# Kernel tuning notes

Hardware: AMD Instinct MI355X
Metric: run time of the kernel (lower is better)

Reference implementation:

```python
import jax, jax.numpy as jnp
import numpy as np

B, H, V = 4096, 2048, 32000
IGNORE_INDEX = -100
BETA = 0.1


def setup_inputs() -> dict:
    key = jax.random.key(0)
    kx, kw, ky = jax.random.split(key, 3)
    x = jax.random.normal(kx, (B, H), dtype=jnp.float32)
    # nn.Linear weight: shape (V, H), uniform(-1/sqrt(H), 1/sqrt(H))
    bound = 1.0 / np.sqrt(H)
    W = jax.random.uniform(kw, (V, H), dtype=jnp.float32, minval=-bound, maxval=bound)
    y = jax.random.randint(ky, (B,), 0, V, dtype=jnp.int64)
    return {"x": x, "W": W, "y": y}


def reference(x, W, y):
    # Linear projection: (B,H) @ (H,V) -> (B,V)
    logits = jnp.einsum("bh,vh->bv", x, W)
    half = logits.shape[0] // 2

    # Cross entropy (mean reduction, ignore_index) on the chosen half.
    logp = jax.nn.log_softmax(logits[:half], axis=-1)  # (half, V)
    y_half = y[:half]
    valid = y_half != IGNORE_INDEX
    safe_y = jnp.where(valid, y_half, 0)
    nll = -jnp.take_along_axis(logp, safe_y[:, None], axis=-1)[:, 0]
    nll = jnp.where(valid, nll, 0.0)
    ce_loss = nll.sum() / jnp.maximum(valid.sum(), 1).astype(nll.dtype)

    # Mean log-prob over the vocab dim for every row (as in the reference).
    all_logprobs = jax.nn.log_softmax(logits, axis=-1).mean(axis=-1)  # (B,)
    chosen = all_logprobs[:half]
    rejected = all_logprobs[half:]

    # ORPO odds-ratio loss
    log_odds = (chosen - rejected) - (
        jnp.log1p(-jnp.exp(chosen)) - jnp.log1p(-jnp.exp(rejected))
    )
    or_losses = BETA * jax.nn.log_sigmoid(log_odds)
    return ce_loss - or_losses.mean()
```

## Files before the change

### kernel.cpp

```cpp
#include <hip/hip_runtime.h>
#include <stdint.h>

#define BDIM 4096
#define HDIM 2048
#define VDIM 32000
#define HALF (BDIM / 2)
#define IGNORE_INDEX (-100)

typedef int   v8i  __attribute__((ext_vector_type(8)));
typedef int   v4i  __attribute__((ext_vector_type(4)));
typedef float v16f __attribute__((ext_vector_type(16)));
typedef float f32x4 __attribute__((ext_vector_type(4)));
typedef __bf16 bf16x8 __attribute__((ext_vector_type(8)));

#define AS1 __attribute__((address_space(1)))
#define AS3 __attribute__((address_space(3)))

__device__ __forceinline__ unsigned short f2bf(float f) {
    union { float f; unsigned int u; } v; v.f = f;
    unsigned int u = v.u;
    unsigned int r = u + 0x7FFFu + ((u >> 16) & 1u);
    return (unsigned short)(r >> 16);
}

__global__ void cvt_fp8_kernel(const float* __restrict__ x,
                               const float* __restrict__ W,
                               uint8_t* __restrict__ xq,
                               uint8_t* __restrict__ wq,
                               int nx16, int ntot16) {
    int stride = gridDim.x * blockDim.x;
    for (int i = blockIdx.x * blockDim.x + threadIdx.x; i < ntot16; i += stride) {
        const float4* s; uint4* d; int j; float m;
        if (i < nx16) { s = (const float4*)x; d = (uint4*)xq; j = i; m = 1.0f; }
        else          { s = (const float4*)W; d = (uint4*)wq; j = i - nx16; m = 64.0f; }
        float4 f0 = s[4 * j + 0], f1 = s[4 * j + 1];
        float4 f2 = s[4 * j + 2], f3 = s[4 * j + 3];
        uint4 o; int w;
        w = __builtin_amdgcn_cvt_pk_fp8_f32(f0.x * m, f0.y * m, 0, false);
        w = __builtin_amdgcn_cvt_pk_fp8_f32(f0.z * m, f0.w * m, w, true);
        o.x = (unsigned)w;
        w = __builtin_amdgcn_cvt_pk_fp8_f32(f1.x * m, f1.y * m, 0, false);
        w = __builtin_amdgcn_cvt_pk_fp8_f32(f1.z * m, f1.w * m, w, true);
        o.y = (unsigned)w;
        w = __builtin_amdgcn_cvt_pk_fp8_f32(f2.x * m, f2.y * m, 0, false);
        w = __builtin_amdgcn_cvt_pk_fp8_f32(f2.z * m, f2.w * m, w, true);
        o.z = (unsigned)w;
        w = __builtin_amdgcn_cvt_pk_fp8_f32(f3.x * m, f3.y * m, 0, false);
        w = __builtin_amdgcn_cvt_pk_fp8_f32(f3.z * m, f3.w * m, w, true);
        o.w = (unsigned)w;
        d[j] = o;
    }
}

__global__ __launch_bounds__(256, 4)
void gemm_reduce_fp8(const uint8_t* __restrict__ A, const uint8_t* __restrict__ B,
                     const int* __restrict__ y,
                     float* __restrict__ sumexp, float* __restrict__ sumlog,
                     float* __restrict__ tlog) {
    __shared__ uint8_t sA[128 * 64];
    __shared__ uint8_t sB[128 * 64];

    const int tid = threadIdx.x;
    const int lane = tid & 63;
    const int wave = tid >> 6;
    const int wm = wave >> 1, wn = wave & 1;
    const int m0 = blockIdx.x * 128;
    const int v0 = blockIdx.y * 128;

    v16f acc[2][2];
#pragma unroll
    for (int i = 0; i < 2; i++)
#pragma unroll
        for (int j = 0; j < 2; j++)
#pragma unroll
            for (int r = 0; r < 16; r++) acc[i][j][r] = 0.f;

    const int srow = wave * 32 + (lane >> 2);
    const int sc   = ((lane & 3) - ((lane >> 3) & 3)) & 3;
    const uint8_t* gA0 = A + (size_t)(m0 + srow) * HDIM + sc * 16;
    const uint8_t* gB0 = B + (size_t)(v0 + srow) * HDIM + sc * 16;
    const uint8_t* gA1 = gA0 + (size_t)16 * HDIM;
    const uint8_t* gB1 = gB0 + (size_t)16 * HDIM;
    uint8_t* lA0 = &sA[(wave * 32) * 64];
    uint8_t* lA1 = lA0 + 16 * 64;
    uint8_t* lB0 = &sB[(wave * 32) * 64];
    uint8_t* lB1 = lB0 + 16 * 64;

    const int fr32 = lane & 31;
    const int h = lane >> 5;
    const int swr = (fr32 >> 1) & 3;
    const int pos0 = (2 * h + swr) & 3;
    const int pos1 = (2 * h + 1 + swr) & 3;
    const v4i* pA0 = (const v4i*)&sA[(wm * 64 + fr32) * 64];
    const v4i* pA1 = (const v4i*)&sA[(wm * 64 + 32 + fr32) * 64];
    const v4i* pB0 = (const v4i*)&sB[(wn * 64 + fr32) * 64];
    const v4i* pB1 = (const v4i*)&sB[(wn * 64 + 32 + fr32) * 64];

    for (int kt = 0; kt < HDIM; kt += 64) {
        __builtin_amdgcn_global_load_lds((const AS1 unsigned int*)(gA0 + kt),
                                         (AS3 unsigned int*)lA0, 16, 0, 0);
        __builtin_amdgcn_global_load_lds((const AS1 unsigned int*)(gA1 + kt),
                                         (AS3 unsigned int*)lA1, 16, 0, 0);
        __builtin_amdgcn_global_load_lds((const AS1 unsigned int*)(gB0 + kt),
                                         (AS3 unsigned int*)lB0, 16, 0, 0);
        __builtin_amdgcn_global_load_lds((const AS1 unsigned int*)(gB1 + kt),
                                         (AS3 unsigned int*)lB1, 16, 0, 0);
        __syncthreads();

        v4i a00 = pA0[pos0], a01 = pA0[pos1];
        v4i a10 = pA1[pos0], a11 = pA1[pos1];
        v4i b00 = pB0[pos0], b01 = pB0[pos1];
        v4i b10 = pB1[pos0], b11 = pB1[pos1];
        v8i af0 = {a00[0], a00[1], a00[2], a00[3], a01[0], a01[1], a01[2], a01[3]};
        v8i af1 = {a10[0], a10[1], a10[2], a10[3], a11[0], a11[1], a11[2], a11[3]};
        v8i bf0 = {b00[0], b00[1], b00[2], b00[3], b01[0], b01[1], b01[2], b01[3]};
        v8i bf1 = {b10[0], b10[1], b10[2], b10[3], b11[0], b11[1], b11[2], b11[3]};

        acc[0][0] = __builtin_amdgcn_mfma_scale_f32_32x32x64_f8f6f4(
            af0, bf0, acc[0][0], 0, 0, 0, 0x7F7F7F7F, 0, 0x7F7F7F7F);
        acc[0][1] = __builtin_amdgcn_mfma_scale_f32_32x32x64_f8f6f4(
            af0, bf1, acc[0][1], 0, 0, 0, 0x7F7F7F7F, 0, 0x7F7F7F7F);
        acc[1][0] = __builtin_amdgcn_mfma_scale_f32_32x32x64_f8f6f4(
            af1, bf0, acc[1][0], 0, 0, 0, 0x7F7F7F7F, 0, 0x7F7F7F7F);
        acc[1][1] = __builtin_amdgcn_mfma_scale_f32_32x32x64_f8f6f4(
            af1, bf1, acc[1][1], 0, 0, 0, 0x7F7F7F7F, 0, 0x7F7F7F7F);
        __syncthreads();
    }

    const float s64 = 0.015625f;
#pragma unroll
    for (int mi = 0; mi < 2; mi++) {
        const int baseRow = m0 + wm * 64 + mi * 32;
#pragma unroll
        for (int reg = 0; reg < 16; reg++) {
            float va = acc[mi][0][reg] * s64;
            float vb = acc[mi][1][reg] * s64;
            float e = __expf(va) + __expf(vb);
            float sm = va + vb;
#pragma unroll
            for (int off = 1; off < 32; off <<= 1) {
                e  += __shfl_xor(e, off);
                sm += __shfl_xor(sm, off);
            }
            int row = baseRow + (reg & 3) + 8 * (reg >> 2) + 4 * h;
            if (fr32 == 0) {
                atomicAdd(&sumexp[row], e);
                atomicAdd(&sumlog[row], sm);
            }
            int yv = y[row];
            int c0 = v0 + wn * 64 + fr32;
            if (c0 == yv) tlog[row] = va;
            if (c0 + 32 == yv) tlog[row] = vb;
        }
    }
}

__global__ __launch_bounds__(256, 4)
void gemm_reduce_f32(const float* __restrict__ A, const float* __restrict__ B,
                     const int* __restrict__ y,
                     float* __restrict__ sumexp, float* __restrict__ sumlog,
                     float* __restrict__ tlog) {
    __shared__ unsigned short sA[128 * 32];
    __shared__ unsigned short sB[128 * 32];

    const int tid  = threadIdx.x;
    const int lane = tid & 63;
    const int wave = tid >> 6;
    const int wm = wave >> 1, wn = wave & 1;
    const int m0 = blockIdx.x * 128;
    const int v0 = blockIdx.y * 128;
    const int fr = lane & 15;
    const int fq = lane >> 4;
    const int swz = (fr >> 1) & 3;

    f32x4 acc[4][4];
#pragma unroll
    for (int i = 0; i < 4; i++)
#pragma unroll
        for (int j = 0; j < 4; j++) acc[i][j] = (f32x4){0.f, 0.f, 0.f, 0.f};

    const int r8 = tid >> 3;
    const int kc = (tid & 7) * 4;
    for (int kt = 0; kt < HDIM; kt += 32) {
#pragma unroll
        for (int p = 0; p < 4; p++) {
            int row = p * 32 + r8;
            int pos = ((kc >> 3) ^ ((row >> 1) & 3)) * 8 + (kc & 7);
            float4 fa = *(const float4*)&A[(size_t)(m0 + row) * HDIM + kt + kc];
            float4 fb = *(const float4*)&B[(size_t)(v0 + row) * HDIM + kt + kc];
            ushort4 ua, ub;
            ua.x = f2bf(fa.x); ua.y = f2bf(fa.y); ua.z = f2bf(fa.z); ua.w = f2bf(fa.w);
            ub.x = f2bf(fb.x); ub.y = f2bf(fb.y); ub.z = f2bf(fb.z); ub.w = f2bf(fb.w);
            *(ushort4*)&sA[row * 32 + pos] = ua;
            *(ushort4*)&sB[row * 32 + pos] = ub;
        }
        __syncthreads();

        bf16x8 af[4], bf[4];
#pragma unroll
        for (int i = 0; i < 4; i++) {
            af[i] = *(const bf16x8*)&sA[(wm * 64 + i * 16 + fr) * 32 + (fq ^ swz) * 8];
            bf[i] = *(const bf16x8*)&sB[(wn * 64 + i * 16 + fr) * 32 + (fq ^ swz) * 8];
        }
#pragma unroll
        for (int mi = 0; mi < 4; mi++)
#pragma unroll
            for (int ni = 0; ni < 4; ni++)
                acc[mi][ni] = __builtin_amdgcn_mfma_f32_16x16x32_bf16(
                    af[mi], bf[ni], acc[mi][ni], 0, 0, 0);
        __syncthreads();
    }

    const int baseRow = m0 + wm * 64;
    const int cbase = v0 + wn * 64 + fr;
#pragma unroll
    for (int mi = 0; mi < 4; mi++) {
        float se[4] = {0.f, 0.f, 0.f, 0.f};
        float sl[4] = {0.f, 0.f, 0.f, 0.f};
#pragma unroll
        for (int ni = 0; ni < 4; ni++)
#pragma unroll
            for (int r = 0; r < 4; r++) {
                float v = acc[mi][ni][r];
                se[r] += __expf(v);
                sl[r] += v;
            }
#pragma unroll
        for (int r = 0; r < 4; r++) {
            float e = se[r], s = sl[r];
#pragma unroll
            for (int off = 1; off < 16; off <<= 1) {
                e += __shfl_xor(e, off);
                s += __shfl_xor(s, off);
            }
            int row = baseRow + mi * 16 + fq * 4 + r;
            if (fr == 0) {
                atomicAdd(&sumexp[row], e);
                atomicAdd(&sumlog[row], s);
            }
            int yv = y[row];
#pragma unroll
            for (int ni = 0; ni < 4; ni++)
                if (cbase + ni * 16 == yv) tlog[row] = acc[mi][ni][r];
        }
    }
}

__global__ void finalize_kernel(const float* __restrict__ sumexp,
                                const float* __restrict__ sumlog,
                                const float* __restrict__ tlog,
                                const int* __restrict__ y,
                                float* __restrict__ out) {
    __shared__ float red[3][4];
    float s_nll = 0.f, s_or = 0.f, cnt = 0.f;
    for (int p = threadIdx.x; p < HALF; p += blockDim.x) {
        float lse_c = logf(sumexp[p]);
        float lse_r = logf(sumexp[p + HALF]);
        float mc = sumlog[p] * (1.0f / VDIM);
        float mr = sumlog[p + HALF] * (1.0f / VDIM);
        int yv = y[p];
        if (yv != IGNORE_INDEX) { s_nll += lse_c - tlog[p]; cnt += 1.f; }
        float ch = mc - lse_c, rj = mr - lse_r;
        float lo = (ch - rj) - (log1pf(-expf(ch)) - log1pf(-expf(rj)));
        float ls = fminf(lo, 0.f) - log1pf(expf(-fabsf(lo)));
        s_or += 0.1f * ls;
    }
    for (int off = 32; off; off >>= 1) {
        s_nll += __shfl_down(s_nll, off);
        s_or  += __shfl_down(s_or, off);
        cnt   += __shfl_down(cnt, off);
    }
    int wave = threadIdx.x >> 6, lane = threadIdx.x & 63;
    if (lane == 0) { red[0][wave] = s_nll; red[1][wave] = s_or; red[2][wave] = cnt; }
    __syncthreads();
    if (threadIdx.x == 0) {
        float tn = 0.f, to = 0.f, tc = 0.f;
        for (int w = 0; w < 4; w++) { tn += red[0][w]; to += red[1][w]; tc += red[2][w]; }
        out[0] = tn / fmaxf(tc, 1.f) - to / (float)HALF;
    }
}

extern "C" void kernel_launch(void* const* d_in, const int* in_sizes, int n_in,
                              void* d_out, int out_size, void* d_ws, size_t ws_size,
                              hipStream_t stream) {
    const float* x = (const float*)d_in[0];
    const float* W = (const float*)d_in[1];
    const int* y   = (const int*)d_in[2];
    float* out     = (float*)d_out;

    float* sumexp = (float*)d_ws;
    float* sumlog = sumexp + BDIM;
    float* tlog   = sumlog + BDIM;
    hipMemsetAsync(d_ws, 0, 3 * BDIM * sizeof(float), stream);

    const size_t bfoff = 65536;
    const size_t xcount = (size_t)BDIM * HDIM;
    const size_t wcount = (size_t)VDIM * HDIM;
    const size_t need = bfoff + xcount + wcount;

    dim3 grid(BDIM / 128, VDIM / 128);
    if (ws_size >= need) {
        uint8_t* xq = (uint8_t*)d_ws + bfoff;
        uint8_t* wq = xq + xcount;
        int nx16 = (int)(xcount / 16);
        int ntot16 = (int)((xcount + wcount) / 16);
        cvt_fp8_kernel<<<4096, 256, 0, stream>>>(x, W, xq, wq, nx16, ntot16);
        gemm_reduce_fp8<<<grid, 256, 0, stream>>>(xq, wq, y, sumexp, sumlog, tlog);
    } else {
        gemm_reduce_f32<<<grid, 256, 0, stream>>>(x, W, y, sumexp, sumlog, tlog);
    }
    finalize_kernel<<<1, 256, 0, stream>>>(sumexp, sumlog, tlog, y, out);
}
```

Before: 818.5 us.

## Double-buffer LDS tiles in FP8 GEMM and flatten conversion kernel grid

The FP8 GEMM mainloop now keeps two 16 KB LDS stages. It issues the global-to-LDS loads for the next K tile after reading fragments from the current one, and drops the trailing barrier. This is meant to overlap memory latency with MFMA work. The cost is twice the LDS use, with the occupancy hint lowered from 4 to 3 blocks per CU. The conversion kernel also changes from a grid-stride loop doing 16 elements per thread to one float4 per thread over a much larger grid.

```diff
diff --git a/kernel.cpp b/kernel.cpp
--- a/kernel.cpp
+++ b/kernel.cpp
@@ -27,38 +27,24 @@
                                const float* __restrict__ W,
                                uint8_t* __restrict__ xq,
                                uint8_t* __restrict__ wq,
-                               int nx16, int ntot16) {
-    int stride = gridDim.x * blockDim.x;
-    for (int i = blockIdx.x * blockDim.x + threadIdx.x; i < ntot16; i += stride) {
-        const float4* s; uint4* d; int j; float m;
-        if (i < nx16) { s = (const float4*)x; d = (uint4*)xq; j = i; m = 1.0f; }
-        else          { s = (const float4*)W; d = (uint4*)wq; j = i - nx16; m = 64.0f; }
-        float4 f0 = s[4 * j + 0], f1 = s[4 * j + 1];
-        float4 f2 = s[4 * j + 2], f3 = s[4 * j + 3];
-        uint4 o; int w;
-        w = __builtin_amdgcn_cvt_pk_fp8_f32(f0.x * m, f0.y * m, 0, false);
-        w = __builtin_amdgcn_cvt_pk_fp8_f32(f0.z * m, f0.w * m, w, true);
-        o.x = (unsigned)w;
-        w = __builtin_amdgcn_cvt_pk_fp8_f32(f1.x * m, f1.y * m, 0, false);
-        w = __builtin_amdgcn_cvt_pk_fp8_f32(f1.z * m, f1.w * m, w, true);
-        o.y = (unsigned)w;
-        w = __builtin_amdgcn_cvt_pk_fp8_f32(f2.x * m, f2.y * m, 0, false);
-        w = __builtin_amdgcn_cvt_pk_fp8_f32(f2.z * m, f2.w * m, w, true);
-        o.z = (unsigned)w;
-        w = __builtin_amdgcn_cvt_pk_fp8_f32(f3.x * m, f3.y * m, 0, false);
-        w = __builtin_amdgcn_cvt_pk_fp8_f32(f3.z * m, f3.w * m, w, true);
-        o.w = (unsigned)w;
-        d[j] = o;
-    }
-}
-
-__global__ __launch_bounds__(256, 4)
+                               int nx4, int ntot4) {
+    int i = blockIdx.x * blockDim.x + threadIdx.x;
+    if (i >= ntot4) return;
+    const float4* s; unsigned* d; int j; float m;
+    if (i < nx4) { s = (const float4*)x; d = (unsigned*)xq; j = i; m = 1.0f; }
+    else         { s = (const float4*)W; d = (unsigned*)wq; j = i - nx4; m = 64.0f; }
+    float4 f = s[j];
+    int w = __builtin_amdgcn_cvt_pk_fp8_f32(f.x * m, f.y * m, 0, false);
+    w = __builtin_amdgcn_cvt_pk_fp8_f32(f.z * m, f.w * m, w, true);
+    d[j] = (unsigned)w;
+}
+
+__global__ __launch_bounds__(256, 3)
 void gemm_reduce_fp8(const uint8_t* __restrict__ A, const uint8_t* __restrict__ B,
                      const int* __restrict__ y,
                      float* __restrict__ sumexp, float* __restrict__ sumlog,
                      float* __restrict__ tlog) {
-    __shared__ uint8_t sA[128 * 64];
-    __shared__ uint8_t sB[128 * 64];
+    __shared__ uint8_t smem[32768];
 
     const int tid = threadIdx.x;
     const int lane = tid & 63;
@@ -77,40 +63,59 @@
 
     const int srow = wave * 32 + (lane >> 2);
     const int sc   = ((lane & 3) - ((lane >> 3) & 3)) & 3;
-    const uint8_t* gA0 = A + (size_t)(m0 + srow) * HDIM + sc * 16;
-    const uint8_t* gB0 = B + (size_t)(v0 + srow) * HDIM + sc * 16;
-    const uint8_t* gA1 = gA0 + (size_t)16 * HDIM;
-    const uint8_t* gB1 = gB0 + (size_t)16 * HDIM;
-    uint8_t* lA0 = &sA[(wave * 32) * 64];
-    uint8_t* lA1 = lA0 + 16 * 64;
-    uint8_t* lB0 = &sB[(wave * 32) * 64];
-    uint8_t* lB1 = lB0 + 16 * 64;
+    const uint8_t* gA = A + (size_t)(m0 + srow) * HDIM + sc * 16;
+    const uint8_t* gB = B + (size_t)(v0 + srow) * HDIM + sc * 16;
+    const int stoff = wave * 2048;
 
     const int fr32 = lane & 31;
     const int h = lane >> 5;
     const int swr = (fr32 >> 1) & 3;
-    const int pos0 = (2 * h + swr) & 3;
-    const int pos1 = (2 * h + 1 + swr) & 3;
-    const v4i* pA0 = (const v4i*)&sA[(wm * 64 + fr32) * 64];
-    const v4i* pA1 = (const v4i*)&sA[(wm * 64 + 32 + fr32) * 64];
-    const v4i* pB0 = (const v4i*)&sB[(wn * 64 + fr32) * 64];
-    const v4i* pB1 = (const v4i*)&sB[(wn * 64 + 32 + fr32) * 64];
-
+    const int p0 = ((2 * h + swr) & 3) * 16;
+    const int p1 = ((2 * h + 1 + swr) & 3) * 16;
+    const int offA = (wm * 64 + fr32) * 64;
+    const int offB = 8192 + (wn * 64 + fr32) * 64;
+
+    {
+        uint8_t* dA = smem + stoff;
+        uint8_t* dB = smem + 8192 + stoff;
+        __builtin_amdgcn_global_load_lds((const AS1 unsigned int*)gA,
+                                         (AS3 unsigned int*)dA, 16, 0, 0);
+        __builtin_amdgcn_global_load_lds((const AS1 unsigned int*)(gA + (size_t)16 * HDIM),
+                                         (AS3 unsigned int*)(dA + 1024), 16, 0, 0);
+        __builtin_amdgcn_global_load_lds((const AS1 unsigned int*)gB,
+                                         (AS3 unsigned int*)dB, 16, 0, 0);
+        __builtin_amdgcn_global_load_lds((const AS1 unsigned int*)(gB + (size_t)16 * HDIM),
+                                         (AS3 unsigned int*)(dB + 1024), 16, 0, 0);
+    }
+
+    int cur = 0;
     for (int kt = 0; kt < HDIM; kt += 64) {
-        __builtin_amdgcn_global_load_lds((const AS1 unsigned int*)(gA0 + kt),
-                                         (AS3 unsigned int*)lA0, 16, 0, 0);
-        __builtin_amdgcn_global_load_lds((const AS1 unsigned int*)(gA1 + kt),
-                                         (AS3 unsigned int*)lA1, 16, 0, 0);
-        __builtin_amdgcn_global_load_lds((const AS1 unsigned int*)(gB0 + kt),
-                                         (AS3 unsigned int*)lB0, 16, 0, 0);
-        __builtin_amdgcn_global_load_lds((const AS1 unsigned int*)(gB1 + kt),
-                                         (AS3 unsigned int*)lB1, 16, 0, 0);
         __syncthreads();
-
-        v4i a00 = pA0[pos0], a01 = pA0[pos1];
-        v4i a10 = pA1[pos0], a11 = pA1[pos1];
-        v4i b00 = pB0[pos0], b01 = pB0[pos1];
-        v4i b10 = pB1[pos0], b11 = pB1[pos1];
+        const uint8_t* base = smem + cur * 16384;
+        v4i a00 = *(const v4i*)(base + offA + p0);
+        v4i a01 = *(const v4i*)(base + offA + p1);
+        v4i a10 = *(const v4i*)(base + offA + 2048 + p0);
+        v4i a11 = *(const v4i*)(base + offA + 2048 + p1);
+        v4i b00 = *(const v4i*)(base + offB + p0);
+        v4i b01 = *(const v4i*)(base + offB + p1);
+        v4i b10 = *(const v4i*)(base + offB + 2048 + p0);
+        v4i b11 = *(const v4i*)(base + offB + 2048 + p1);
+
+        if (kt + 64 < HDIM) {
+            uint8_t* dA = smem + (cur ^ 1) * 16384 + stoff;
+            uint8_t* dB = smem + (cur ^ 1) * 16384 + 8192 + stoff;
+            const uint8_t* sgA = gA + kt + 64;
+            const uint8_t* sgB = gB + kt + 64;
+            __builtin_amdgcn_global_load_lds((const AS1 unsigned int*)sgA,
+                                             (AS3 unsigned int*)dA, 16, 0, 0);
+            __builtin_amdgcn_global_load_lds((const AS1 unsigned int*)(sgA + (size_t)16 * HDIM),
+                                             (AS3 unsigned int*)(dA + 1024), 16, 0, 0);
+            __builtin_amdgcn_global_load_lds((const AS1 unsigned int*)sgB,
+                                             (AS3 unsigned int*)dB, 16, 0, 0);
+            __builtin_amdgcn_global_load_lds((const AS1 unsigned int*)(sgB + (size_t)16 * HDIM),
+                                             (AS3 unsigned int*)(dB + 1024), 16, 0, 0);
+        }
+
         v8i af0 = {a00[0], a00[1], a00[2], a00[3], a01[0], a01[1], a01[2], a01[3]};
         v8i af1 = {a10[0], a10[1], a10[2], a10[3], a11[0], a11[1], a11[2], a11[3]};
         v8i bf0 = {b00[0], b00[1], b00[2], b00[3], b01[0], b01[1], b01[2], b01[3]};
@@ -124,7 +129,8 @@
             af1, bf0, acc[1][0], 0, 0, 0, 0x7F7F7F7F, 0, 0x7F7F7F7F);
         acc[1][1] = __builtin_amdgcn_mfma_scale_f32_32x32x64_f8f6f4(
             af1, bf1, acc[1][1], 0, 0, 0, 0x7F7F7F7F, 0, 0x7F7F7F7F);
-        __syncthreads();
+
+        cur ^= 1;
     }
 
     const float s64 = 0.015625f;
@@ -302,9 +308,9 @@
     if (ws_size >= need) {
         uint8_t* xq = (uint8_t*)d_ws + bfoff;
         uint8_t* wq = xq + xcount;
-        int nx16 = (int)(xcount / 16);
-        int ntot16 = (int)((xcount + wcount) / 16);
-        cvt_fp8_kernel<<<4096, 256, 0, stream>>>(x, W, xq, wq, nx16, ntot16);
+        int nx4 = (int)(xcount / 4);
+        int ntot4 = (int)((xcount + wcount) / 4);
+        cvt_fp8_kernel<<<(ntot4 + 255) / 256, 256, 0, stream>>>(x, W, xq, wq, nx4, ntot4);
         gemm_reduce_fp8<<<grid, 256, 0, stream>>>(xq, wq, y, sumexp, sumlog, tlog);
     } else {
         gemm_reduce_f32<<<grid, 256, 0, stream>>>(x, W, y, sumexp, sumlog, tlog);
```

Result: slower. 2.849 ms (+248.1%).
